# Kernel optimization log

Hardware: AMD Instinct MI355X
Metric: run time of the kernel (lower is better)

The kernel has to match this reference:

```python
import jax, jax.numpy as jnp
import numpy as np

DIM = 1024
HEADS = 16
DIM_HEAD = 64
DIM_INNER = HEADS * DIM_HEAD  # 1024
SEQ = 2048
BATCH = 1


def setup_inputs() -> dict:
    key = jax.random.key(0)
    k1, k2, k3 = jax.random.split(key, 3)
    x = jax.random.normal(k1, (BATCH, SEQ, DIM), dtype=jnp.float32)
    # LinearNoBias(dim, 6*dim_inner): stored as [dim, 6*dim_inner] so fwd is x @ W
    W_qkv = jax.random.normal(k2, (DIM, 6 * DIM_INNER), dtype=jnp.float32) * (DIM ** -0.5)
    W_out = jax.random.normal(k3, (DIM_INNER, DIM), dtype=jnp.float32) * (DIM_INNER ** -0.5)
    return {"x": x, "W_qkv": W_qkv, "W_out": W_out}


def reference(x, W_qkv, W_out):
    b, n, _ = x.shape
    scale = DIM_HEAD ** -0.5

    qkv = x @ W_qkv  # [b, n, 6*h*d]
    qkv = qkv.reshape(b, n, 6, HEADS, DIM_HEAD).transpose(2, 0, 3, 1, 4)  # [6, b, h, n, d]
    qu, ku, vu, qc, kc, vc = qkv

    qc_s = qc * scale
    qu_s = qu * scale

    # strictly-upper-triangular causal mask (True above diagonal)
    causal_mask = jnp.triu(jnp.ones((n, n), dtype=bool), 1)

    # term1: lower-triangular (incl. diag) of qc_s @ vu^T
    term1 = jnp.einsum('bhid,bhjd->bhij', qc_s, vu)
    term1 = jnp.where(causal_mask, 0.0, term1)

    # lookahead: sigmoid of qu_s @ ku^T, strictly upper kept
    lookahead = jax.nn.sigmoid(jnp.einsum('bhid,bhjd->bhij', qu_s, ku))
    lookahead = jnp.where(causal_mask, lookahead, 0.0)

    # Su = term1 @ lookahead^T  (n x n by n x n matmul per head)
    Su = jnp.einsum('bhij,bhkj->bhik', term1, lookahead)

    Sc = jnp.einsum('bhid,bhjd->bhij', qc_s, kc)
    scores = Sc - jax.nn.silu(Su)
    scores = jnp.where(causal_mask, -jnp.inf, scores)

    attn = jax.nn.softmax(scores, axis=-1)
    out = jnp.einsum('bhij,bhjd->bhid', attn, vc)  # [b, h, n, d]

    out = out.transpose(0, 2, 1, 3).reshape(b, n, DIM_INNER)
    return out @ W_out
```

## Files before the change

### kernel.cpp

```cpp
#include <hip/hip_runtime.h>
#include <math.h>

typedef _Float16 f16;
typedef _Float16 f16x4 __attribute__((ext_vector_type(4)));
typedef _Float16 f16x8 __attribute__((ext_vector_type(8)));
typedef float f32x4 __attribute__((ext_vector_type(4)));

#define SEQ   2048
#define DIM   1024
#define NH    16
#define DH    64
#define NCOLS 6144
#define NHSD  (NH*SEQ*DH)
#define NTILE 136
#define MAXS  9
#define SLOTS_PER_HEAD 64

__device__ __forceinline__ int ns2(int a) {
  const int NS2[8] = {1,1,2,3,4,5,7,9};
  return NS2[a];
}
__device__ __forceinline__ int slot_base(int I) {
  const int PF[16] = {0,1,2,3,4,6,8,11,14,18,22,27,32,39,46,55};
  return PF[I];
}

__global__ __launch_bounds__(256) void k_tcast(const float* __restrict__ in, f16* __restrict__ out,
                                               int R, int C) {
  __shared__ f16 t[64 * 66];
  int bc = blockIdx.x, br = blockIdx.y;
  for (int it = 0; it < 16; ++it) {
    int idx = it * 256 + threadIdx.x;
    int r = idx >> 6, c = idx & 63;
    t[r * 66 + c] = (f16)in[(size_t)(br * 64 + r) * C + bc * 64 + c];
  }
  __syncthreads();
  for (int it = 0; it < 16; ++it) {
    int idx = it * 256 + threadIdx.x;
    int oc = idx >> 6, orr = idx & 63;
    out[(size_t)(bc * 64 + oc) * R + br * 64 + orr] = t[orr * 66 + oc];
  }
}

__global__ __launch_bounds__(256) void k_prepA(const float* __restrict__ x, f16* __restrict__ xhT) {
  int kt = blockIdx.x, by = blockIdx.y;
  f16* dst = xhT + ((size_t)(by * 16 + kt) << 13);
  int tid = threadIdx.x;
#pragma unroll
  for (int i = 0; i < 4; ++i) {
    int idx = i * 256 + tid;
    int chunk = idx >> 6, lane = idx & 63;
    int rb = chunk & 7, ks = chunk >> 3;
    int row = by * 128 + rb * 16 + (lane & 15);
    int kk = kt * 64 + ks * 32 + ((lane >> 4) << 3);
    const float* p = x + (size_t)row * DIM + kk;
    float4 lo = *(const float4*)p, hi = *(const float4*)(p + 4);
    f16x8 h;
    h[0] = (f16)lo.x; h[1] = (f16)lo.y; h[2] = (f16)lo.z; h[3] = (f16)lo.w;
    h[4] = (f16)hi.x; h[5] = (f16)hi.y; h[6] = (f16)hi.z; h[7] = (f16)hi.w;
    *(f16x8*)(dst + (size_t)idx * 8) = h;
  }
}

__global__ __launch_bounds__(256) void k_prepB(const float* __restrict__ Wq, f16* __restrict__ WqTf) {
  int kt = blockIdx.x, bx = blockIdx.y;
  f16* dst = WqTf + ((size_t)(bx * 16 + kt) << 13);
  int tid = threadIdx.x;
#pragma unroll
  for (int i = 0; i < 4; ++i) {
    int idx = i * 256 + tid;
    int chunk = idx >> 6, lane = idx & 63;
    int rb = chunk & 7, ks = chunk >> 3;
    int n = bx * 128 + rb * 16 + (lane & 15);
    int kk = kt * 64 + ks * 32 + ((lane >> 4) << 3);
    f16x8 h;
#pragma unroll
    for (int j = 0; j < 8; ++j) h[j] = (f16)Wq[(size_t)(kk + j) * NCOLS + n];
    *(f16x8*)(dst + (size_t)idx * 8) = h;
  }
}

__global__ __launch_bounds__(256) void k_gemm_qkv(const f16* __restrict__ xhT, const f16* __restrict__ WqTf,
                                                  f16* __restrict__ q6, f16* __restrict__ vuF) {
  __shared__ f16 sa[8192];
  __shared__ f16 sb[8192];
  int bx = blockIdx.x, by = blockIdx.y;
  int tid = threadIdx.x, w = tid >> 6, l = tid & 63, q = l >> 4, c = l & 15;
  f32x4 acc[2][8];
  const f32x4 zf = {0.f, 0.f, 0.f, 0.f};
  for (int i = 0; i < 2; ++i) for (int j = 0; j < 8; ++j) acc[i][j] = zf;

  for (int kt = 0; kt < 16; ++kt) {
    const f16* ta = xhT + ((size_t)(by * 16 + kt) << 13);
    const f16* tb = WqTf + ((size_t)(bx * 16 + kt) << 13);
    __syncthreads();
#pragma unroll
    for (int i = 0; i < 4; ++i) {
      int e = (i * 256 + tid) * 8;
      __builtin_amdgcn_global_load_lds((const __attribute__((address_space(1))) void*)(ta + e),
                                       (__attribute__((address_space(3))) void*)(sa + e), 16, 0, 0);
      __builtin_amdgcn_global_load_lds((const __attribute__((address_space(1))) void*)(tb + e),
                                       (__attribute__((address_space(3))) void*)(sb + e), 16, 0, 0);
    }
    __syncthreads();
#pragma unroll
    for (int ks = 0; ks < 2; ++ks) {
      f16x8 af[2], bf[8];
#pragma unroll
      for (int tr = 0; tr < 2; ++tr)
        af[tr] = *(const f16x8*)(sa + ((ks * 8 + w * 2 + tr) * 64 + l) * 8);
#pragma unroll
      for (int tc = 0; tc < 8; ++tc)
        bf[tc] = *(const f16x8*)(sb + ((ks * 8 + tc) * 64 + l) * 8);
#pragma unroll
      for (int tr = 0; tr < 2; ++tr)
#pragma unroll
        for (int tc = 0; tc < 8; ++tc)
          acc[tr][tc] = __builtin_amdgcn_mfma_f32_16x16x32_f16(af[tr], bf[tc], acc[tr][tc], 0, 0, 0);
    }
  }
#pragma unroll
  for (int tr = 0; tr < 2; ++tr)
#pragma unroll
    for (int tc = 0; tc < 8; ++tc)
#pragma unroll
      for (int r = 0; r < 4; ++r) {
        int row = by * 128 + w * 32 + tr * 16 + q * 4 + r;
        int col = bx * 128 + tc * 16 + c;
        float v = acc[tr][tc][r];
        int t = col >> 10, head = (col >> 6) & 15, dh = col & 63;
        if (t == 0 || t == 3) v *= 0.125f;
        f16 hv = (f16)v;
        if (t == 4) {
          size_t addr = (size_t)4 * NHSD + (size_t)head * (SEQ * DH) + ((size_t)(row >> 7) << 13)
                      + (size_t)(((((dh >> 5) << 3) + ((row >> 4) & 7)) * 64
                                  + ((((dh >> 3) & 3) << 4) | (row & 15))) * 8 + (dh & 7));
          q6[addr] = hv;
        } else if (t == 5) {
          size_t addr = (size_t)5 * NHSD + (size_t)head * (SEQ * DH) + ((size_t)(row >> 7) << 13)
                      + (size_t)((((((row >> 5) & 3) << 2) + (dh >> 4)) * 64
                                  + ((((row >> 3) & 3) << 4) | (dh & 15))) * 8 + (row & 7));
          q6[addr] = hv;
        } else if (t == 2) {
          q6[(size_t)2 * NHSD + (size_t)(head * SEQ + row) * DH + dh] = hv;
          size_t fa = ((size_t)(row >> 7) << 13)
                    + (size_t)((((((row >> 5) & 3) << 2) + (dh >> 4)) * 64
                                + ((((row >> 3) & 3) << 4) | (dh & 15))) * 8 + (row & 7));
          vuF[(size_t)head * (SEQ * DH) + fa] = hv;
        } else {
          q6[(size_t)t * NHSD + (size_t)(head * SEQ + row) * DH + dh] = hv;
        }
      }
}

__global__ __launch_bounds__(256) void k_t1lk(const f16* __restrict__ q6, f16* __restrict__ t1dT,
                                              f16* __restrict__ lkT) {
  __shared__ f16 st[128 * 128];
  int head = blockIdx.x / 152;
  int p = blockIdx.x % 152;
  bool is_lk = (p >= 16);
  int RB, CB;
  f16* dst;
  if (is_lk) {
    int p2 = p - 16;
    int K = 0, off = 0;
    while (off + (16 - K) <= p2) { off += 16 - K; ++K; }
    RB = K; CB = K + (p2 - off);
    dst = lkT + ((size_t)(head * NTILE + p2) << 14);
  } else {
    RB = p; CB = p;
    dst = t1dT + ((size_t)(head * 16 + p) << 14);
  }
  const f16* Ah = q6 + (size_t)(is_lk ? 0 : 3) * NHSD + (size_t)head * SEQ * DH;
  const f16* Bh = q6 + (size_t)(is_lk ? 1 : 2) * NHSD + (size_t)head * SEQ * DH;
  int tid = threadIdx.x, w = tid >> 6, l = tid & 63, q = l >> 4, c = l & 15;
  const f32x4 zf = {0.f, 0.f, 0.f, 0.f};
  f32x4 tacc[2][8];
  for (int tr = 0; tr < 2; ++tr) for (int tc = 0; tc < 8; ++tc) tacc[tr][tc] = zf;
#pragma unroll
  for (int ks = 0; ks < 2; ++ks) {
    f16x8 aq[2], bf[8];
#pragma unroll
    for (int tr = 0; tr < 2; ++tr)
      aq[tr] = *(const f16x8*)(Ah + (size_t)(RB * 128 + w * 32 + tr * 16 + c) * DH + ks * 32 + q * 8);
#pragma unroll
    for (int tc = 0; tc < 8; ++tc)
      bf[tc] = *(const f16x8*)(Bh + (size_t)(CB * 128 + tc * 16 + c) * DH + ks * 32 + q * 8);
#pragma unroll
    for (int tr = 0; tr < 2; ++tr)
#pragma unroll
      for (int tc = 0; tc < 8; ++tc)
        tacc[tr][tc] = __builtin_amdgcn_mfma_f32_16x16x32_f16(aq[tr], bf[tc], tacc[tr][tc], 0, 0, 0);
  }
#pragma unroll
  for (int tr = 0; tr < 2; ++tr)
#pragma unroll
    for (int tc = 0; tc < 8; ++tc)
#pragma unroll
      for (int r = 0; r < 4; ++r) {
        int row = w * 32 + tr * 16 + q * 4 + r;
        int col = tc * 16 + c;
        int rg = RB * 128 + row, cg = CB * 128 + col;
        float v = tacc[tr][tc][r];
        f16 ov;
        if (is_lk) ov = (cg > rg) ? (f16)__builtin_amdgcn_rcpf(1.f + __expf(-v)) : (f16)(0.f);
        else       ov = (cg <= rg) ? (f16)v : (f16)(0.f);
        st[(row << 7) + (((col >> 3) ^ (row & 15)) << 3) + (col & 7)] = ov;
      }
  __syncthreads();
#pragma unroll
  for (int i = 0; i < 8; ++i) {
    int ch = i * 256 + tid;
    int ks = ch >> 9, rb = (ch >> 6) & 7, ln = ch & 63;
    int qq = ln >> 4, cc = ln & 15;
    int row = rb * 16 + cc, cchunk = ks * 4 + qq;
    f16x8 v = *(const f16x8*)(st + (row << 7) + ((cchunk ^ (row & 15)) << 3));
    *(f16x8*)(dst + (size_t)ch * 8) = v;
  }
}

__global__ __launch_bounds__(256) void k_prefix(const f16* __restrict__ lkT, const f16* __restrict__ vuF,
                                                f16* __restrict__ PPT) {
  __shared__ f16 lkb[2][16384];
  __shared__ f16 vub[2][8192];
  __shared__ f16 st[8192];
  int head = blockIdx.x >> 4, K = blockIdx.x & 15;
  int offK = 16 * K - (K * (K - 1)) / 2;
  const f16* lkh = lkT + ((size_t)(head * NTILE) << 14);
  const f16* vuh = vuF + (size_t)head * (SEQ * DH);
  f16* pph = PPT + ((size_t)(head * NTILE) << 13);
  int tid = threadIdx.x, w = tid >> 6, l = tid & 63, q = l >> 4, c = l & 15;
  f32x4 acc[2][4];
  const f32x4 zf = {0.f, 0.f, 0.f, 0.f};
  for (int tr = 0; tr < 2; ++tr) for (int tv = 0; tv < 4; ++tv) acc[tr][tv] = zf;
  {
    const f16* lt = lkh + ((size_t)offK << 14);
#pragma unroll
    for (int i = 0; i < 8; ++i) {
      int e = (i * 256 + tid) * 8;
      __builtin_amdgcn_global_load_lds((const __attribute__((address_space(1))) void*)(lt + e),
                                       (__attribute__((address_space(3))) void*)(&lkb[0][0] + e), 16, 0, 0);
    }
    const f16* vt_ = vuh + ((size_t)K << 13);
#pragma unroll
    for (int i = 0; i < 4; ++i) {
      int e = (i * 256 + tid) * 8;
      __builtin_amdgcn_global_load_lds((const __attribute__((address_space(1))) void*)(vt_ + e),
                                       (__attribute__((address_space(3))) void*)(&vub[0][0] + e), 16, 0, 0);
    }
  }
  int pb = 0;
  for (int J = K; J < 16; ++J) {
    __syncthreads();
    if (J < 15) {
      const f16* lt = lkh + ((size_t)(offK + (J + 1 - K)) << 14);
#pragma unroll
      for (int i = 0; i < 8; ++i) {
        int e = (i * 256 + tid) * 8;
        __builtin_amdgcn_global_load_lds((const __attribute__((address_space(1))) void*)(lt + e),
                                         (__attribute__((address_space(3))) void*)(&lkb[pb ^ 1][0] + e), 16, 0, 0);
      }
      const f16* vt_ = vuh + ((size_t)(J + 1) << 13);
#pragma unroll
      for (int i = 0; i < 4; ++i) {
        int e = (i * 256 + tid) * 8;
        __builtin_amdgcn_global_load_lds((const __attribute__((address_space(1))) void*)(vt_ + e),
                                         (__attribute__((address_space(3))) void*)(&vub[pb ^ 1][0] + e), 16, 0, 0);
      }
    }
#pragma unroll
    for (int ks = 0; ks < 4; ++ks) {
      f16x8 af[2], bf[4];
#pragma unroll
      for (int tr = 0; tr < 2; ++tr)
        af[tr] = *(const f16x8*)(&lkb[pb][0] + ((ks * 8 + w * 2 + tr) * 64 + l) * 8);
#pragma unroll
      for (int tv = 0; tv < 4; ++tv)
        bf[tv] = *(const f16x8*)(&vub[pb][0] + ((ks * 4 + tv) * 64 + l) * 8);
#pragma unroll
      for (int tr = 0; tr < 2; ++tr)
#pragma unroll
        for (int tv = 0; tv < 4; ++tv)
          acc[tr][tv] = __builtin_amdgcn_mfma_f32_16x16x32_f16(af[tr], bf[tv], acc[tr][tv], 0, 0, 0);
    }
#pragma unroll
    for (int tr = 0; tr < 2; ++tr)
#pragma unroll
      for (int tv = 0; tv < 4; ++tv)
#pragma unroll
        for (int r = 0; r < 4; ++r) {
          int row = w * 32 + tr * 16 + q * 4 + r;
          int col = tv * 16 + c;
          st[(row << 6) + (((col >> 3) ^ (row & 7)) << 3) + (col & 7)] = (f16)acc[tr][tv][r];
        }
    __syncthreads();
    f16* dst = pph + ((size_t)(offK + (J - K)) << 13);
#pragma unroll
    for (int i = 0; i < 4; ++i) {
      int slot = i * 256 + tid;
      int chunk = slot >> 6, ln = slot & 63;
      int ks2 = chunk >> 3, tc = chunk & 7, qq = ln >> 4, cc = ln & 15;
      int row = tc * 16 + cc, cch = ks2 * 4 + qq;
      f16x8 v = *(const f16x8*)(st + (row << 6) + ((cch ^ (row & 7)) << 3));
      *(f16x8*)(dst + (size_t)slot * 8) = v;
    }
    pb ^= 1;
  }
}

__global__ __launch_bounds__(256, 1) void k_flash(const f16* __restrict__ q6, const f16* __restrict__ t1dT,
                                                  const f16* __restrict__ lkT, const f16* __restrict__ PPT,
                                                  f16* __restrict__ pO, float* __restrict__ pML) {
  __shared__ f16 Sb[2][40960];
  int bid = blockIdx.x;
  int big = bid & 1;
  int rest = bid >> 1;
  int head = ((rest & 7) << 1) | ((rest >> 3) & 1);
  int r2 = 31 - (rest >> 4);
  int a = 0, s = 0;
  {
    int acc = 0;
    for (int aa = 0; aa < 8; ++aa) {
      int si = ns2(aa);
      if (r2 >= acc && r2 < acc + si) { a = aa; s = r2 - acc; }
      acc += si;
    }
  }
  int I1 = 2 * a + 1;
  int S_ = ns2(a);
  int Ktot = I1 + 1;
  int K0 = (Ktot * s) / S_, K1 = (Ktot * (s + 1)) / S_;
  int IB = 2 * a + big;
  int Kbeg = (K0 < IB + 1) ? K0 : IB + 1;
  int Kend = (K1 < IB + 1) ? K1 : IB + 1;

  const f16* qc  = q6 + (size_t)3 * NHSD + (size_t)head * SEQ * DH;
  const f16* kcF = q6 + (size_t)4 * NHSD + (size_t)head * (SEQ * DH);
  const f16* vtF = q6 + (size_t)5 * NHSD + (size_t)head * (SEQ * DH);
  int tid = threadIdx.x, w = tid >> 6, l = tid & 63, q = l >> 4, c = l & 15;
  int wi = w;
  const f16* lkh = lkT + ((size_t)(head * NTILE) << 14);
  const f16* pph = PPT + ((size_t)(head * NTILE) << 13);
  const f16* t1d = t1dT + ((size_t)(head * 16 + IB) << 14);

  f16x8 a_qc[2][2];
#pragma unroll
  for (int tr = 0; tr < 2; ++tr)
#pragma unroll
    for (int ks = 0; ks < 2; ++ks)
      a_qc[tr][ks] = *(const f16x8*)(qc + (size_t)(IB * 128 + wi * 32 + tr * 16 + c) * DH + ks * 32 + q * 8);
  f16x8 a_t1[4][2];
#pragma unroll
  for (int ks = 0; ks < 4; ++ks)
#pragma unroll
    for (int tr = 0; tr < 2; ++tr)
      a_t1[ks][tr] = *(const f16x8*)(t1d + (size_t)((ks * 8 + wi * 2 + tr) * 64 + l) * 8);

  f32x4 su[2][8], oacc[2][4];
  float m_i[2][4], l_i[2][4];
  const f32x4 zf = {0.f, 0.f, 0.f, 0.f};
  for (int tr = 0; tr < 2; ++tr) for (int tv = 0; tv < 4; ++tv) oacc[tr][tv] = zf;
  for (int tr = 0; tr < 2; ++tr) for (int r = 0; r < 4; ++r) { m_i[tr][r] = -INFINITY; l_i[tr][r] = 0.f; }

  if (Kbeg < Kend) {
    int K = Kbeg;
    int offK = 16 * K - (K * (K - 1)) / 2;
    f16* D = &Sb[0][0];
    const f16* p1 = lkh + ((size_t)(offK + (IB - K)) << 14);
#pragma unroll
    for (int i = 0; i < 8; ++i) {
      int e = (i * 256 + tid) * 8;
      __builtin_amdgcn_global_load_lds((const __attribute__((address_space(1))) void*)(p1 + e),
                                       (__attribute__((address_space(3))) void*)(D + e), 16, 0, 0);
    }
    if (K < IB) {
      const f16* pp = pph + ((size_t)(offK + (IB - 1 - K)) << 13);
#pragma unroll
      for (int i = 0; i < 4; ++i) {
        int e = (i * 256 + tid) * 8;
        __builtin_amdgcn_global_load_lds((const __attribute__((address_space(1))) void*)(pp + e),
                                         (__attribute__((address_space(3))) void*)(D + 16384 + e), 16, 0, 0);
      }
    }
    const f16* kt_ = kcF + ((size_t)K << 13);
    const f16* vv_ = vtF + ((size_t)K << 13);
#pragma unroll
    for (int i = 0; i < 4; ++i) {
      int e = (i * 256 + tid) * 8;
      __builtin_amdgcn_global_load_lds((const __attribute__((address_space(1))) void*)(kt_ + e),
                                       (__attribute__((address_space(3))) void*)(D + 24576 + e), 16, 0, 0);
      __builtin_amdgcn_global_load_lds((const __attribute__((address_space(1))) void*)(vv_ + e),
                                       (__attribute__((address_space(3))) void*)(D + 32768 + e), 16, 0, 0);
    }
  }

  int cur = 0;
  for (int K = Kbeg; K < Kend; ++K) {
#pragma unroll
    for (int tr = 0; tr < 2; ++tr) for (int tc = 0; tc < 8; ++tc) su[tr][tc] = zf;

    __syncthreads();

    if (K + 1 < Kend) {
      int Kn = K + 1;
      int offKn = 16 * Kn - (Kn * (Kn - 1)) / 2;
      f16* D = &Sb[cur ^ 1][0];
      const f16* p1 = lkh + ((size_t)(offKn + (IB - Kn)) << 14);
#pragma unroll
      for (int i = 0; i < 8; ++i) {
        int e = (i * 256 + tid) * 8;
        __builtin_amdgcn_global_load_lds((const __attribute__((address_space(1))) void*)(p1 + e),
                                         (__attribute__((address_space(3))) void*)(D + e), 16, 0, 0);
      }
      if (Kn < IB) {
        const f16* pp = pph + ((size_t)(offKn + (IB - 1 - Kn)) << 13);
#pragma unroll
        for (int i = 0; i < 4; ++i) {
          int e = (i * 256 + tid) * 8;
          __builtin_amdgcn_global_load_lds((const __attribute__((address_space(1))) void*)(pp + e),
                                           (__attribute__((address_space(3))) void*)(D + 16384 + e), 16, 0, 0);
        }
      }
      const f16* kt_ = kcF + ((size_t)Kn << 13);
      const f16* vv_ = vtF + ((size_t)Kn << 13);
#pragma unroll
      for (int i = 0; i < 4; ++i) {
        int e = (i * 256 + tid) * 8;
        __builtin_amdgcn_global_load_lds((const __attribute__((address_space(1))) void*)(kt_ + e),
                                         (__attribute__((address_space(3))) void*)(D + 24576 + e), 16, 0, 0);
        __builtin_amdgcn_global_load_lds((const __attribute__((address_space(1))) void*)(vv_ + e),
                                         (__attribute__((address_space(3))) void*)(D + 32768 + e), 16, 0, 0);
      }
    }

    f16* bufc = &Sb[cur][0];
    if (K < IB) {
      const f16* ppb = bufc + 16384;
#pragma unroll
      for (int ks = 0; ks < 2; ++ks) {
        f16x8 bf[8];
#pragma unroll
        for (int tc = 0; tc < 8; ++tc)
          bf[tc] = *(const f16x8*)(ppb + ((ks * 8 + tc) * 64 + l) * 8);
#pragma unroll
        for (int tr = 0; tr < 2; ++tr)
#pragma unroll
          for (int tc = 0; tc < 8; ++tc)
            su[tr][tc] = __builtin_amdgcn_mfma_f32_16x16x32_f16(a_qc[tr][ks], bf[tc], su[tr][tc], 0, 0, 0);
      }
    }
    {
      __builtin_amdgcn_s_setprio(1);
#pragma unroll
      for (int ks = 0; ks < 4; ++ks) {
        f16x8 bf[8];
#pragma unroll
        for (int tc = 0; tc < 8; ++tc)
          bf[tc] = *(const f16x8*)(bufc + ((ks * 8 + tc) * 64 + l) * 8);
#pragma unroll
        for (int tr = 0; tr < 2; ++tr)
#pragma unroll
          for (int tc = 0; tc < 8; ++tc)
            su[tr][tc] = __builtin_amdgcn_mfma_f32_16x16x32_f16(a_t1[ks][tr], bf[tc], su[tr][tc], 0, 0, 0);
      }
      __builtin_amdgcn_s_setprio(0);
    }
#pragma unroll
    for (int tr = 0; tr < 2; ++tr)
#pragma unroll
      for (int tc = 0; tc < 8; ++tc)
#pragma unroll
        for (int r = 0; r < 4; ++r) {
          float v = su[tr][tc][r];
          su[tr][tc][r] = -v * __builtin_amdgcn_rcpf(1.f + __expf(-v));
        }
    {
      const f16* skc = bufc + 24576;
#pragma unroll
      for (int ks = 0; ks < 2; ++ks) {
        f16x8 bk[8];
#pragma unroll
        for (int tc = 0; tc < 8; ++tc)
          bk[tc] = *(const f16x8*)(skc + ((ks * 8 + tc) * 64 + l) * 8);
#pragma unroll
        for (int tr = 0; tr < 2; ++tr)
#pragma unroll
          for (int tc = 0; tc < 8; ++tc)
            su[tr][tc] = __builtin_amdgcn_mfma_f32_16x16x32_f16(a_qc[tr][ks], bk[tc], su[tr][tc], 0, 0, 0);
      }
    }
    if (K == IB) {
#pragma unroll
      for (int tr = 0; tr < 2; ++tr)
#pragma unroll
        for (int tc = 0; tc < 8; ++tc)
#pragma unroll
          for (int r = 0; r < 4; ++r) {
            int rg = wi * 32 + tr * 16 + q * 4 + r;
            int cg = tc * 16 + c;
            if (cg > rg) su[tr][tc][r] = -INFINITY;
          }
    }
#pragma unroll
    for (int tr = 0; tr < 2; ++tr)
#pragma unroll
      for (int r = 0; r < 4; ++r) {
        float mx = su[tr][0][r];
#pragma unroll
        for (int tc = 1; tc < 8; ++tc) mx = fmaxf(mx, su[tr][tc][r]);
        mx = fmaxf(mx, __shfl_xor(mx, 1)); mx = fmaxf(mx, __shfl_xor(mx, 2));
        mx = fmaxf(mx, __shfl_xor(mx, 4)); mx = fmaxf(mx, __shfl_xor(mx, 8));
        float mnew  = fmaxf(m_i[tr][r], mx);
        float alpha = __expf(m_i[tr][r] - mnew);
        float ssum = 0.f;
#pragma unroll
        for (int tc = 0; tc < 8; ++tc) {
          float pp = __expf(su[tr][tc][r] - mnew);
          su[tr][tc][r] = pp;
          ssum += pp;
        }
        ssum += __shfl_xor(ssum, 1); ssum += __shfl_xor(ssum, 2);
        ssum += __shfl_xor(ssum, 4); ssum += __shfl_xor(ssum, 8);
        l_i[tr][r] = l_i[tr][r] * alpha + ssum;
        m_i[tr][r] = mnew;
#pragma unroll
        for (int tv = 0; tv < 4; ++tv) oacc[tr][tv][r] *= alpha;
      }
    asm volatile("s_waitcnt lgkmcnt(0)" ::: "memory");
    __builtin_amdgcn_sched_barrier(0);
    __builtin_amdgcn_s_barrier();
    __builtin_amdgcn_sched_barrier(0);
#pragma unroll
    for (int tr = 0; tr < 2; ++tr)
#pragma unroll
      for (int tc = 0; tc < 8; ++tc)
#pragma unroll
        for (int r = 0; r < 4; ++r) {
          int row = w * 32 + tr * 16 + q * 4 + r;
          int col = tc * 16 + c;
          bufc[(row << 7) + (((col >> 3) ^ (row & 15)) << 3) + (col & 7)] = (f16)su[tr][tc][r];
        }
    {
      const f16* svt = bufc + 32768;
#pragma unroll
      for (int ks = 0; ks < 4; ++ks) {
        int ck = ks * 4 + q;
        f16x8 ap[2], bv[4];
#pragma unroll
        for (int tr = 0; tr < 2; ++tr)
          ap[tr] = *(const f16x8*)(bufc + ((w * 32 + tr * 16 + c) << 7) + ((ck ^ c) << 3));
#pragma unroll
        for (int tv = 0; tv < 4; ++tv)
          bv[tv] = *(const f16x8*)(svt + ((ks * 4 + tv) * 64 + l) * 8);
#pragma unroll
        for (int tr = 0; tr < 2; ++tr)
#pragma unroll
          for (int tv = 0; tv < 4; ++tv)
            oacc[tr][tv] = __builtin_amdgcn_mfma_f32_16x16x32_f16(ap[tr], bv[tv], oacc[tr][tv], 0, 0, 0);
      }
    }
    cur ^= 1;
  }

  int slot = head * SLOTS_PER_HEAD + slot_base(IB) + s;
  f16* po = pO + (size_t)slot * (128 * 64);
  float* pml = pML + (size_t)slot * 256;
  if (c == 0) {
#pragma unroll
    for (int tr = 0; tr < 2; ++tr)
#pragma unroll
      for (int r = 0; r < 4; ++r) {
        int row = wi * 32 + tr * 16 + q * 4 + r;
        pml[row] = m_i[tr][r];
        pml[128 + row] = l_i[tr][r];
      }
  }
#pragma unroll
  for (int tr = 0; tr < 2; ++tr)
#pragma unroll
    for (int tv = 0; tv < 4; ++tv)
#pragma unroll
      for (int r = 0; r < 4; ++r) {
        int row = wi * 32 + tr * 16 + q * 4 + r;
        int col = tv * 16 + c;
        po[row * 64 + col] = (f16)oacc[tr][tv][r];
      }
}

__global__ __launch_bounds__(256) void k_merge(const f16* __restrict__ pO, const float* __restrict__ pML,
                                               f16* __restrict__ oh) {
  int head = blockIdx.x >> 4, I = blockIdx.x & 15;
  int S_ = ns2(I >> 1);
  int tid = threadIdx.x;
  int row = tid >> 1, half = tid & 1;
  int base = head * SLOTS_PER_HEAD + slot_base(I);
  float m[MAXS], lv[MAXS];
  float mstar = -INFINITY;
#pragma unroll
  for (int s = 0; s < MAXS; ++s)
    if (s < S_) {
      m[s] = pML[(size_t)(base + s) * 256 + row];
      lv[s] = pML[(size_t)(base + s) * 256 + 128 + row];
      mstar = fmaxf(mstar, m[s]);
    }
  float wt[MAXS];
  float lsum = 0.f;
#pragma unroll
  for (int s = 0; s < MAXS; ++s)
    if (s < S_) {
      wt[s] = __expf(m[s] - mstar);
      lsum += lv[s] * wt[s];
    }
  float rinv = __builtin_amdgcn_rcpf(lsum);
#pragma unroll
  for (int cc = 0; cc < 32; cc += 8) {
    float acc[8] = {0.f, 0.f, 0.f, 0.f, 0.f, 0.f, 0.f, 0.f};
#pragma unroll
    for (int s = 0; s < MAXS; ++s)
      if (s < S_) {
        f16x8 v = *(const f16x8*)(pO + (size_t)(base + s) * 8192 + row * 64 + half * 32 + cc);
#pragma unroll
        for (int e = 0; e < 8; ++e) acc[e] += wt[s] * (float)v[e];
      }
    f16x8 o;
#pragma unroll
    for (int e = 0; e < 8; ++e) o[e] = (f16)(acc[e] * rinv);
    *(f16x8*)(oh + (size_t)(I * 128 + row) * DIM + head * 64 + half * 32 + cc) = o;
  }
}

__global__ __launch_bounds__(256) void k_gemm_out(const f16* __restrict__ A, const f16* __restrict__ B,
                                                  float* __restrict__ out) {
  __shared__ f16 sa[128 * 72];
  __shared__ f16 sb[128 * 72];
  int bx = blockIdx.x, by = blockIdx.y;
  int tid = threadIdx.x, w = tid >> 6, l = tid & 63, q = l >> 4, c = l & 15;
  f32x4 acc[2][8];
  const f32x4 zf = {0.f, 0.f, 0.f, 0.f};
  for (int i = 0; i < 2; ++i) for (int j = 0; j < 8; ++j) acc[i][j] = zf;
  for (int kt = 0; kt < DIM / 64; ++kt) {
    __syncthreads();
#pragma unroll
    for (int it = 0; it < 4; ++it) {
      int idx = it * 256 + tid; int r = idx >> 3, ch = idx & 7;
      *(float4*)(sa + r * 72 + ch * 8) = *(const float4*)(A + (size_t)(by * 128 + r) * DIM + kt * 64 + ch * 8);
      *(float4*)(sb + r * 72 + ch * 8) = *(const float4*)(B + (size_t)(bx * 128 + r) * DIM + kt * 64 + ch * 8);
    }
    __syncthreads();
#pragma unroll
    for (int ks = 0; ks < 2; ++ks) {
      f16x8 af[2], bf[8];
#pragma unroll
      for (int tr = 0; tr < 2; ++tr) af[tr] = *(const f16x8*)(sa + (w * 32 + tr * 16 + c) * 72 + ks * 32 + q * 8);
#pragma unroll
      for (int tc = 0; tc < 8; ++tc) bf[tc] = *(const f16x8*)(sb + (tc * 16 + c) * 72 + ks * 32 + q * 8);
#pragma unroll
      for (int tr = 0; tr < 2; ++tr)
#pragma unroll
        for (int tc = 0; tc < 8; ++tc)
          acc[tr][tc] = __builtin_amdgcn_mfma_f32_16x16x32_f16(af[tr], bf[tc], acc[tr][tc], 0, 0, 0);
    }
  }
#pragma unroll
  for (int tr = 0; tr < 2; ++tr)
#pragma unroll
    for (int tc = 0; tc < 8; ++tc)
#pragma unroll
      for (int r = 0; r < 4; ++r) {
        int row = by * 128 + w * 32 + tr * 16 + q * 4 + r;
        int col = bx * 128 + tc * 16 + c;
        out[(size_t)row * DIM + col] = acc[tr][tc][r];
      }
}

extern "C" void kernel_launch(void* const* d_in, const int* in_sizes, int n_in,
                              void* d_out, int out_size, void* d_ws, size_t ws_size,
                              hipStream_t stream) {
  const float* x  = (const float*)d_in[0];
  const float* Wq = (const float*)d_in[1];
  const float* Wo = (const float*)d_in[2];
  float* out = (float*)d_out;

  f16* ws = (f16*)d_ws;
  size_t off = 0;
  f16* q6   = ws + off; off += (size_t)6 * NHSD;
  f16* vuF  = ws + off; off += (size_t)NHSD;
  f16* xhT  = ws + off; off += (size_t)SEQ * DIM;
  f16* WqTf = ws + off; off += (size_t)NCOLS * DIM;
  f16* WoT  = ws + off; off += (size_t)DIM * DIM;
  f16* oh   = ws + off; off += (size_t)SEQ * DIM;
  f16* pO   = ws + off; off += (size_t)NH * SLOTS_PER_HEAD * 128 * 64;
  f16* lkT  = ws + off; off += (size_t)NH * NTILE * 128 * 128;
  f16* t1dT = ws + off; off += (size_t)NH * 16 * 128 * 128;
  f16* PPT  = ws + off; off += (size_t)NH * NTILE * 128 * 64;
  float* pML = (float*)(ws + off); off += (size_t)NH * SLOTS_PER_HEAD * 256 * 2;

  k_prepA<<<dim3(16, 16), 256, 0, stream>>>(x, xhT);
  k_prepB<<<dim3(16, 48), 256, 0, stream>>>(Wq, WqTf);
  k_tcast<<<dim3(DIM / 64, DIM / 64), 256, 0, stream>>>(Wo, WoT, DIM, DIM);
  k_gemm_qkv<<<dim3(NCOLS / 128, SEQ / 128), 256, 0, stream>>>(xhT, WqTf, q6, vuF);
  k_t1lk<<<NH * 152, 256, 0, stream>>>(q6, t1dT, lkT);
  k_prefix<<<NH * 16, 256, 0, stream>>>(lkT, vuF, PPT);
  k_flash<<<NH * 64, 256, 0, stream>>>(q6, t1dT, lkT, PPT, pO, pML);
  k_merge<<<NH * 16, 256, 0, stream>>>(pO, pML, oh);
  k_gemm_out<<<dim3(DIM / 128, SEQ / 128), 256, 0, stream>>>(oh, WoT, out);
}
```

Before: 340.1 us.

## Split flash kernel work across 8 waves with 16 rows each instead of 4 waves

The k_flash kernel now launches 512 threads (8 waves) per block, and each wave owns 16 query rows instead of 32. Per-wave register arrays (su, oacc, a_qc, a_t1, softmax state) are halved, and the cooperative LDS loads are redistributed over 512 threads. The aim is more latency hiding and lower register pressure per wave for the same LDS footprint. In exchange, each wave reuses each B fragment loaded from LDS for half as many MFMAs, so LDS read traffic per FLOP doubles, and barrier costs span more waves.

```diff
diff --git a/kernel.cpp b/kernel.cpp
--- a/kernel.cpp
+++ b/kernel.cpp
@@ -308,7 +308,7 @@
   }
 }
 
-__global__ __launch_bounds__(256, 1) void k_flash(const f16* __restrict__ q6, const f16* __restrict__ t1dT,
+__global__ __launch_bounds__(512, 1) void k_flash(const f16* __restrict__ q6, const f16* __restrict__ t1dT,
                                                   const f16* __restrict__ lkT, const f16* __restrict__ PPT,
                                                   f16* __restrict__ pO, float* __restrict__ pML) {
   __shared__ f16 Sb[2][40960];
@@ -338,29 +338,24 @@
   const f16* kcF = q6 + (size_t)4 * NHSD + (size_t)head * (SEQ * DH);
   const f16* vtF = q6 + (size_t)5 * NHSD + (size_t)head * (SEQ * DH);
   int tid = threadIdx.x, w = tid >> 6, l = tid & 63, q = l >> 4, c = l & 15;
-  int wi = w;
   const f16* lkh = lkT + ((size_t)(head * NTILE) << 14);
   const f16* pph = PPT + ((size_t)(head * NTILE) << 13);
   const f16* t1d = t1dT + ((size_t)(head * 16 + IB) << 14);
 
-  f16x8 a_qc[2][2];
-#pragma unroll
-  for (int tr = 0; tr < 2; ++tr)
-#pragma unroll
-    for (int ks = 0; ks < 2; ++ks)
-      a_qc[tr][ks] = *(const f16x8*)(qc + (size_t)(IB * 128 + wi * 32 + tr * 16 + c) * DH + ks * 32 + q * 8);
-  f16x8 a_t1[4][2];
+  f16x8 a_qc[2];
+#pragma unroll
+  for (int ks = 0; ks < 2; ++ks)
+    a_qc[ks] = *(const f16x8*)(qc + (size_t)(IB * 128 + w * 16 + c) * DH + ks * 32 + q * 8);
+  f16x8 a_t1[4];
 #pragma unroll
   for (int ks = 0; ks < 4; ++ks)
-#pragma unroll
-    for (int tr = 0; tr < 2; ++tr)
-      a_t1[ks][tr] = *(const f16x8*)(t1d + (size_t)((ks * 8 + wi * 2 + tr) * 64 + l) * 8);
-
-  f32x4 su[2][8], oacc[2][4];
-  float m_i[2][4], l_i[2][4];
+    a_t1[ks] = *(const f16x8*)(t1d + (size_t)((ks * 8 + w) * 64 + l) * 8);
+
+  f32x4 su[8], oacc[4];
+  float m_i[4], l_i[4];
   const f32x4 zf = {0.f, 0.f, 0.f, 0.f};
-  for (int tr = 0; tr < 2; ++tr) for (int tv = 0; tv < 4; ++tv) oacc[tr][tv] = zf;
-  for (int tr = 0; tr < 2; ++tr) for (int r = 0; r < 4; ++r) { m_i[tr][r] = -INFINITY; l_i[tr][r] = 0.f; }
+  for (int tv = 0; tv < 4; ++tv) oacc[tv] = zf;
+  for (int r = 0; r < 4; ++r) { m_i[r] = -INFINITY; l_i[r] = 0.f; }
 
   if (Kbeg < Kend) {
     int K = Kbeg;
@@ -368,16 +363,16 @@
     f16* D = &Sb[0][0];
     const f16* p1 = lkh + ((size_t)(offK + (IB - K)) << 14);
 #pragma unroll
-    for (int i = 0; i < 8; ++i) {
-      int e = (i * 256 + tid) * 8;
+    for (int i = 0; i < 4; ++i) {
+      int e = (i * 512 + tid) * 8;
       __builtin_amdgcn_global_load_lds((const __attribute__((address_space(1))) void*)(p1 + e),
                                        (__attribute__((address_space(3))) void*)(D + e), 16, 0, 0);
     }
     if (K < IB) {
       const f16* pp = pph + ((size_t)(offK + (IB - 1 - K)) << 13);
 #pragma unroll
-      for (int i = 0; i < 4; ++i) {
-        int e = (i * 256 + tid) * 8;
+      for (int i = 0; i < 2; ++i) {
+        int e = (i * 512 + tid) * 8;
         __builtin_amdgcn_global_load_lds((const __attribute__((address_space(1))) void*)(pp + e),
                                          (__attribute__((address_space(3))) void*)(D + 16384 + e), 16, 0, 0);
       }
@@ -385,8 +380,8 @@
     const f16* kt_ = kcF + ((size_t)K << 13);
     const f16* vv_ = vtF + ((size_t)K << 13);
 #pragma unroll
-    for (int i = 0; i < 4; ++i) {
-      int e = (i * 256 + tid) * 8;
+    for (int i = 0; i < 2; ++i) {
+      int e = (i * 512 + tid) * 8;
       __builtin_amdgcn_global_load_lds((const __attribute__((address_space(1))) void*)(kt_ + e),
                                        (__attribute__((address_space(3))) void*)(D + 24576 + e), 16, 0, 0);
       __builtin_amdgcn_global_load_lds((const __attribute__((address_space(1))) void*)(vv_ + e),
@@ -397,7 +392,7 @@
   int cur = 0;
   for (int K = Kbeg; K < Kend; ++K) {
 #pragma unroll
-    for (int tr = 0; tr < 2; ++tr) for (int tc = 0; tc < 8; ++tc) su[tr][tc] = zf;
+    for (int tc = 0; tc < 8; ++tc) su[tc] = zf;
 
     __syncthreads();
 
@@ -407,16 +402,16 @@
       f16* D = &Sb[cur ^ 1][0];
       const f16* p1 = lkh + ((size_t)(offKn + (IB - Kn)) << 14);
 #pragma unroll
-      for (int i = 0; i < 8; ++i) {
-        int e = (i * 256 + tid) * 8;
+      for (int i = 0; i < 4; ++i) {
+        int e = (i * 512 + tid) * 8;
         __builtin_amdgcn_global_load_lds((const __attribute__((address_space(1))) void*)(p1 + e),
                                          (__attribute__((address_space(3))) void*)(D + e), 16, 0, 0);
       }
       if (Kn < IB) {
         const f16* pp = pph + ((size_t)(offKn + (IB - 1 - Kn)) << 13);
 #pragma unroll
-        for (int i = 0; i < 4; ++i) {
-          int e = (i * 256 + tid) * 8;
+        for (int i = 0; i < 2; ++i) {
+          int e = (i * 512 + tid) * 8;
           __builtin_amdgcn_global_load_lds((const __attribute__((address_space(1))) void*)(pp + e),
                                            (__attribute__((address_space(3))) void*)(D + 16384 + e), 16, 0, 0);
         }
@@ -424,8 +419,8 @@
       const f16* kt_ = kcF + ((size_t)Kn << 13);
       const f16* vv_ = vtF + ((size_t)Kn << 13);
 #pragma unroll
-      for (int i = 0; i < 4; ++i) {
-        int e = (i * 256 + tid) * 8;
+      for (int i = 0; i < 2; ++i) {
+        int e = (i * 512 + tid) * 8;
         __builtin_amdgcn_global_load_lds((const __attribute__((address_space(1))) void*)(kt_ + e),
                                          (__attribute__((address_space(3))) void*)(D + 24576 + e), 16, 0, 0);
         __builtin_amdgcn_global_load_lds((const __attribute__((address_space(1))) void*)(vv_ + e),
@@ -443,10 +438,8 @@
         for (int tc = 0; tc < 8; ++tc)
           bf[tc] = *(const f16x8*)(ppb + ((ks * 8 + tc) * 64 + l) * 8);
 #pragma unroll
-        for (int tr = 0; tr < 2; ++tr)
-#pragma unroll
-          for (int tc = 0; tc < 8; ++tc)
-            su[tr][tc] = __builtin_amdgcn_mfma_f32_16x16x32_f16(a_qc[tr][ks], bf[tc], su[tr][tc], 0, 0, 0);
+        for (int tc = 0; tc < 8; ++tc)
+          su[tc] = __builtin_amdgcn_mfma_f32_16x16x32_f16(a_qc[ks], bf[tc], su[tc], 0, 0, 0);
       }
     }
     {
@@ -458,22 +451,18 @@
         for (int tc = 0; tc < 8; ++tc)
           bf[tc] = *(const f16x8*)(bufc + ((ks * 8 + tc) * 64 + l) * 8);
 #pragma unroll
-        for (int tr = 0; tr < 2; ++tr)
-#pragma unroll
-          for (int tc = 0; tc < 8; ++tc)
-            su[tr][tc] = __builtin_amdgcn_mfma_f32_16x16x32_f16(a_t1[ks][tr], bf[tc], su[tr][tc], 0, 0, 0);
+        for (int tc = 0; tc < 8; ++tc)
+          su[tc] = __builtin_amdgcn_mfma_f32_16x16x32_f16(a_t1[ks], bf[tc], su[tc], 0, 0, 0);
       }
       __builtin_amdgcn_s_setprio(0);
     }
 #pragma unroll
-    for (int tr = 0; tr < 2; ++tr)
-#pragma unroll
-      for (int tc = 0; tc < 8; ++tc)
-#pragma unroll
-        for (int r = 0; r < 4; ++r) {
-          float v = su[tr][tc][r];
-          su[tr][tc][r] = -v * __builtin_amdgcn_rcpf(1.f + __expf(-v));
-        }
+    for (int tc = 0; tc < 8; ++tc)
+#pragma unroll
+      for (int r = 0; r < 4; ++r) {
+        float v = su[tc][r];
+        su[tc][r] = -v * __builtin_amdgcn_rcpf(1.f + __expf(-v));
+      }
     {
       const f16* skc = bufc + 24576;
 #pragma unroll
@@ -483,80 +472,68 @@
         for (int tc = 0; tc < 8; ++tc)
           bk[tc] = *(const f16x8*)(skc + ((ks * 8 + tc) * 64 + l) * 8);
 #pragma unroll
-        for (int tr = 0; tr < 2; ++tr)
-#pragma unroll
-          for (int tc = 0; tc < 8; ++tc)
-            su[tr][tc] = __builtin_amdgcn_mfma_f32_16x16x32_f16(a_qc[tr][ks], bk[tc], su[tr][tc], 0, 0, 0);
+        for (int tc = 0; tc < 8; ++tc)
+          su[tc] = __builtin_amdgcn_mfma_f32_16x16x32_f16(a_qc[ks], bk[tc], su[tc], 0, 0, 0);
       }
     }
     if (K == IB) {
 #pragma unroll
-      for (int tr = 0; tr < 2; ++tr)
-#pragma unroll
-        for (int tc = 0; tc < 8; ++tc)
-#pragma unroll
-          for (int r = 0; r < 4; ++r) {
-            int rg = wi * 32 + tr * 16 + q * 4 + r;
-            int cg = tc * 16 + c;
-            if (cg > rg) su[tr][tc][r] = -INFINITY;
-          }
-    }
-#pragma unroll
-    for (int tr = 0; tr < 2; ++tr)
-#pragma unroll
-      for (int r = 0; r < 4; ++r) {
-        float mx = su[tr][0][r];
-#pragma unroll
-        for (int tc = 1; tc < 8; ++tc) mx = fmaxf(mx, su[tr][tc][r]);
-        mx = fmaxf(mx, __shfl_xor(mx, 1)); mx = fmaxf(mx, __shfl_xor(mx, 2));
-        mx = fmaxf(mx, __shfl_xor(mx, 4)); mx = fmaxf(mx, __shfl_xor(mx, 8));
-        float mnew  = fmaxf(m_i[tr][r], mx);
-        float alpha = __expf(m_i[tr][r] - mnew);
-        float ssum = 0.f;
-#pragma unroll
-        for (int tc = 0; tc < 8; ++tc) {
-          float pp = __expf(su[tr][tc][r] - mnew);
-          su[tr][tc][r] = pp;
-          ssum += pp;
+      for (int tc = 0; tc < 8; ++tc)
+#pragma unroll
+        for (int r = 0; r < 4; ++r) {
+          int rg = w * 16 + q * 4 + r;
+          int cg = tc * 16 + c;
+          if (cg > rg) su[tc][r] = -INFINITY;
         }
-        ssum += __shfl_xor(ssum, 1); ssum += __shfl_xor(ssum, 2);
-        ssum += __shfl_xor(ssum, 4); ssum += __shfl_xor(ssum, 8);
-        l_i[tr][r] = l_i[tr][r] * alpha + ssum;
-        m_i[tr][r] = mnew;
-#pragma unroll
-        for (int tv = 0; tv < 4; ++tv) oacc[tr][tv][r] *= alpha;
-      }
+    }
+#pragma unroll
+    for (int r = 0; r < 4; ++r) {
+      float mx = su[0][r];
+#pragma unroll
+      for (int tc = 1; tc < 8; ++tc) mx = fmaxf(mx, su[tc][r]);
+      mx = fmaxf(mx, __shfl_xor(mx, 1)); mx = fmaxf(mx, __shfl_xor(mx, 2));
+      mx = fmaxf(mx, __shfl_xor(mx, 4)); mx = fmaxf(mx, __shfl_xor(mx, 8));
+      float mnew  = fmaxf(m_i[r], mx);
+      float alpha = __expf(m_i[r] - mnew);
+      float ssum = 0.f;
+#pragma unroll
+      for (int tc = 0; tc < 8; ++tc) {
+        float pp = __expf(su[tc][r] - mnew);
+        su[tc][r] = pp;
+        ssum += pp;
+      }
+      ssum += __shfl_xor(ssum, 1); ssum += __shfl_xor(ssum, 2);
+      ssum += __shfl_xor(ssum, 4); ssum += __shfl_xor(ssum, 8);
+      l_i[r] = l_i[r] * alpha + ssum;
+      m_i[r] = mnew;
+#pragma unroll
+      for (int tv = 0; tv < 4; ++tv) oacc[tv][r] *= alpha;
+    }
     asm volatile("s_waitcnt lgkmcnt(0)" ::: "memory");
     __builtin_amdgcn_sched_barrier(0);
     __builtin_amdgcn_s_barrier();
     __builtin_amdgcn_sched_barrier(0);
 #pragma unroll
-    for (int tr = 0; tr < 2; ++tr)
-#pragma unroll
-      for (int tc = 0; tc < 8; ++tc)
-#pragma unroll
-        for (int r = 0; r < 4; ++r) {
-          int row = w * 32 + tr * 16 + q * 4 + r;
-          int col = tc * 16 + c;
-          bufc[(row << 7) + (((col >> 3) ^ (row & 15)) << 3) + (col & 7)] = (f16)su[tr][tc][r];
-        }
+    for (int tc = 0; tc < 8; ++tc)
+#pragma unroll
+      for (int r = 0; r < 4; ++r) {
+        int row = w * 16 + q * 4 + r;
+        int col = tc * 16 + c;
+        bufc[(row << 7) + (((col >> 3) ^ (row & 15)) << 3) + (col & 7)] = (f16)su[tc][r];
+      }
     {
       const f16* svt = bufc + 32768;
 #pragma unroll
       for (int ks = 0; ks < 4; ++ks) {
         int ck = ks * 4 + q;
-        f16x8 ap[2], bv[4];
-#pragma unroll
-        for (int tr = 0; tr < 2; ++tr)
-          ap[tr] = *(const f16x8*)(bufc + ((w * 32 + tr * 16 + c) << 7) + ((ck ^ c) << 3));
+        f16x8 ap, bv[4];
+        ap = *(const f16x8*)(bufc + ((w * 16 + c) << 7) + ((ck ^ c) << 3));
 #pragma unroll
         for (int tv = 0; tv < 4; ++tv)
           bv[tv] = *(const f16x8*)(svt + ((ks * 4 + tv) * 64 + l) * 8);
 #pragma unroll
-        for (int tr = 0; tr < 2; ++tr)
-#pragma unroll
-          for (int tv = 0; tv < 4; ++tv)
-            oacc[tr][tv] = __builtin_amdgcn_mfma_f32_16x16x32_f16(ap[tr], bv[tv], oacc[tr][tv], 0, 0, 0);
+        for (int tv = 0; tv < 4; ++tv)
+          oacc[tv] = __builtin_amdgcn_mfma_f32_16x16x32_f16(ap, bv[tv], oacc[tv], 0, 0, 0);
       }
     }
     cur ^= 1;
@@ -567,24 +544,20 @@
   float* pml = pML + (size_t)slot * 256;
   if (c == 0) {
 #pragma unroll
-    for (int tr = 0; tr < 2; ++tr)
-#pragma unroll
-      for (int r = 0; r < 4; ++r) {
-        int row = wi * 32 + tr * 16 + q * 4 + r;
-        pml[row] = m_i[tr][r];
-        pml[128 + row] = l_i[tr][r];
-      }
-  }
-#pragma unroll
-  for (int tr = 0; tr < 2; ++tr)
-#pragma unroll
-    for (int tv = 0; tv < 4; ++tv)
-#pragma unroll
-      for (int r = 0; r < 4; ++r) {
-        int row = wi * 32 + tr * 16 + q * 4 + r;
-        int col = tv * 16 + c;
-        po[row * 64 + col] = (f16)oacc[tr][tv][r];
-      }
+    for (int r = 0; r < 4; ++r) {
+      int row = w * 16 + q * 4 + r;
+      pml[row] = m_i[r];
+      pml[128 + row] = l_i[r];
+    }
+  }
+#pragma unroll
+  for (int tv = 0; tv < 4; ++tv)
+#pragma unroll
+    for (int r = 0; r < 4; ++r) {
+      int row = w * 16 + q * 4 + r;
+      int col = tv * 16 + c;
+      po[row * 64 + col] = (f16)oacc[tv][r];
+    }
 }
 
 __global__ __launch_bounds__(256) void k_merge(const f16* __restrict__ pO, const float* __restrict__ pML,
@@ -701,7 +674,7 @@
   k_gemm_qkv<<<dim3(NCOLS / 128, SEQ / 128), 256, 0, stream>>>(xhT, WqTf, q6, vuF);
   k_t1lk<<<NH * 152, 256, 0, stream>>>(q6, t1dT, lkT);
   k_prefix<<<NH * 16, 256, 0, stream>>>(lkT, vuF, PPT);
-  k_flash<<<NH * 64, 256, 0, stream>>>(q6, t1dT, lkT, PPT, pO, pML);
+  k_flash<<<NH * 64, 512, 0, stream>>>(q6, t1dT, lkT, PPT, pO, pML);
   k_merge<<<NH * 16, 256, 0, stream>>>(pO, pML, oh);
   k_gemm_out<<<dim3(DIM / 128, SEQ / 128), 256, 0, stream>>>(oh, WoT, out);
 }
```

Result: faster. 315.2 us (-7.3%).
